# Kernel optimization log

Hardware: AMD Instinct MI355X
Metric: run time of the kernel (lower is better)

Reference implementation:

```python
import jax, jax.numpy as jnp
import numpy as np

N = 131072      # 8192 sudoku puzzles x 16 cells
E = 1048576     # random constraint edges (avg degree 8)
HID = 64
NEG_SLOPE = 0.2


def setup_inputs() -> dict:
    key = jax.random.key(0)
    ks = jax.random.split(key, 18)
    p = lambda k, shape: jax.random.normal(k, shape, dtype=jnp.float32) * 0.05
    return {
        "x": jax.random.randint(ks[0], (N,), 0, 5),
        "edge_index": jax.random.randint(ks[1], (2, E), 0, N),
        "emb": p(ks[2], (5, HID)),
        # conv1: in 64 -> heads=4, C=64, concat
        "W1": p(ks[3], (HID, 4 * HID)),
        "a1_src": p(ks[4], (4, HID)),
        "a1_dst": p(ks[5], (4, HID)),
        "b1": p(ks[6], (4 * HID,)),
        # conv2: in 256 -> heads=4, C=64, concat
        "W2": p(ks[7], (4 * HID, 4 * HID)),
        "a2_src": p(ks[8], (4, HID)),
        "a2_dst": p(ks[9], (4, HID)),
        "b2": p(ks[10], (4 * HID,)),
        # conv3: in 256 -> heads=1, C=64, no concat
        "W3": p(ks[11], (4 * HID, HID)),
        "a3_src": p(ks[12], (1, HID)),
        "a3_dst": p(ks[13], (1, HID)),
        "b3": p(ks[14], (HID,)),
        "fc_w": p(ks[15], (HID, 5)),
        "fc_b": p(ks[16], (5,)),
    }


def gat_conv(x, src, dst, W, a_src, a_dst, b, concat):
    """PyG-style GATConv (self-loops already appended to src/dst)."""
    n = x.shape[0]
    H, C = a_src.shape
    h = (x @ W).reshape(n, H, C)                       # [N,H,C]
    alpha_s = jnp.einsum('nhc,hc->nh', h, a_src)       # [N,H]
    alpha_d = jnp.einsum('nhc,hc->nh', h, a_dst)
    e = jax.nn.leaky_relu(alpha_s[src] + alpha_d[dst], NEG_SLOPE)  # [E,H]
    # scatter-softmax over incoming edges per destination node
    e_max = jax.ops.segment_max(e, dst, num_segments=n)
    e_exp = jnp.exp(e - e_max[dst])
    denom = jax.ops.segment_sum(e_exp, dst, num_segments=n)
    alpha = e_exp / (denom[dst] + 1e-16)               # [E,H]
    msg = h[src] * alpha[:, :, None]                   # [E,H,C]
    out = jax.ops.segment_sum(msg, dst, num_segments=n)  # [N,H,C]
    out = out.reshape(n, H * C) if concat else out.mean(axis=1)
    return out + b


def reference(x, edge_index, emb, W1, a1_src, a1_dst, b1,
              W2, a2_src, a2_dst, b2, W3, a3_src, a3_dst, b3, fc_w, fc_b):
    n = x.shape[0]
    loops = jnp.arange(n)
    src = jnp.concatenate([edge_index[0], loops])  # add self-loops (PyG default)
    dst = jnp.concatenate([edge_index[1], loops])
    h = emb[x]                                                    # [N,64]
    h = jax.nn.elu(gat_conv(h, src, dst, W1, a1_src, a1_dst, b1, True))
    h = jax.nn.elu(gat_conv(h, src, dst, W2, a2_src, a2_dst, b2, True))
    h = jax.nn.elu(gat_conv(h, src, dst, W3, a3_src, a3_dst, b3, False))
    return h @ fc_w + fc_b                                        # [N,5]
```

## Files before the change

### kernel.cpp

```cpp
#include <hip/hip_runtime.h>
#include <hip/hip_bf16.h>
#include <hip/hip_fp8.h>

typedef __attribute__((ext_vector_type(8))) short short8;
typedef __attribute__((ext_vector_type(4))) short short4_t;
typedef __attribute__((ext_vector_type(4))) float floatx4;
typedef __attribute__((ext_vector_type(2))) float floatx2;

constexpr int NB  = 256;
constexpr int CAP = 6144;

__device__ __forceinline__ unsigned short f2bf(float f){
  unsigned int u = __float_as_uint(f);
  u += 0x7FFF + ((u >> 16) & 1);
  return (unsigned short)(u >> 16);
}
__device__ __forceinline__ float bf2f(unsigned short h){
  return __uint_as_float(((unsigned int)h) << 16);
}
__device__ __forceinline__ float lrelu(float x){ return x > 0.f ? x : 0.2f * x; }
__device__ __forceinline__ float eluf(float x){ return x > 0.f ? x : (__expf(x) - 1.f); }

__device__ __forceinline__ unsigned char f2fp8(float f){
  __hip_fp8_e4m3 t(f);
  return (unsigned char)t.__x;
}
__device__ __forceinline__ float fp82f(unsigned char b){
  __hip_fp8_e4m3 t;
  t.__x = (__hip_fp8_storage_t)b;
  return (float)t;
}

template<bool HI>
__device__ __forceinline__ floatx2 fp8pk2(unsigned int v){
#if defined(__has_builtin) && __has_builtin(__builtin_amdgcn_cvt_pk_f32_fp8)
  return __builtin_amdgcn_cvt_pk_f32_fp8((int)v, HI);
#else
  floatx2 r;
  constexpr int sh = HI ? 16 : 0;
  r.x = fp82f((unsigned char)((v >> sh) & 0xFF));
  r.y = fp82f((unsigned char)((v >> (sh + 8)) & 0xFF));
  return r;
#endif
}

__device__ __forceinline__ unsigned int f32x4_to_fp8(float a0, float a1, float a2, float a3){
#if defined(__has_builtin) && __has_builtin(__builtin_amdgcn_cvt_pk_fp8_f32)
  int w = 0;
  w = __builtin_amdgcn_cvt_pk_fp8_f32(a0, a1, w, false);
  w = __builtin_amdgcn_cvt_pk_fp8_f32(a2, a3, w, true);
  return (unsigned int)w;
#else
  return (unsigned int)f2fp8(a0) | ((unsigned int)f2fp8(a1) << 8) |
         ((unsigned int)f2fp8(a2) << 16) | ((unsigned int)f2fp8(a3) << 24);
#endif
}

__device__ __forceinline__ int scr512(int p){
  int c = p >> 4, s = p & 15;
  int cc = ((c & 7) << 2) | (c >> 3);
  return (cc << 4) | s;
}

__device__ __forceinline__ void gload16(const unsigned short* g, unsigned short* l){
  __builtin_amdgcn_global_load_lds(
      (const __attribute__((address_space(1))) unsigned int*)(const void*)g,
      (__attribute__((address_space(3))) unsigned int*)(void*)l,
      16, 0, 0);
}

__global__ __launch_bounds__(256) void part_prep_k(const int* __restrict__ ei, int E, int shift,
                                                   const int* __restrict__ x,
                                                   int* __restrict__ gcnt,
                                                   unsigned* __restrict__ bbuf, int PB,
                                                   const float* __restrict__ W2,
                                                   unsigned short* __restrict__ Wp2,
                                                   const float* __restrict__ W3,
                                                   unsigned short* __restrict__ Wp3,
                                                   const float* __restrict__ emb,
                                                   const float* __restrict__ W1,
                                                   const float* __restrict__ a1s,
                                                   const float* __restrict__ a1d,
                                                   float* __restrict__ T1,
                                                   float* __restrict__ wt_tab){
  int blk = blockIdx.x;
  int tid = threadIdx.x;
  if (blk < PB){
    __shared__ int hist[NB];
    __shared__ int base[NB];
    hist[tid] = 0;
    __syncthreads();
    int blk_start = blk * 4096;
    int ldmask = (1 << shift) - 1;
    unsigned word[16];
    int bkt[16], lp[16];
    #pragma unroll
    for (int k = 0; k < 16; k++){
      int i = blk_start + k * 256 + tid;
      if (i < E){
        int dst = ei[E + i];
        int s = ei[i];
        int xs = x[s];
        bkt[k] = dst >> shift;
        word[k] = (unsigned)s | ((unsigned)(dst & ldmask) << 17) | ((unsigned)xs << 26);
        lp[k] = atomicAdd(&hist[bkt[k]], 1);
      } else {
        bkt[k] = -1;
      }
    }
    __syncthreads();
    base[tid] = atomicAdd(&gcnt[tid], hist[tid]);
    __syncthreads();
    #pragma unroll
    for (int k = 0; k < 16; k++){
      if (bkt[k] >= 0){
        int b = bkt[k];
        bbuf[(size_t)b * CAP + base[b] + lp[k]] = word[k];
      }
    }
    return;
  }
  int b = blk - PB;
  if (b < 256){
    int idx = b * 256 + tid;
    int k = idx >> 8, nn = idx & 255;
    Wp2[nn * 256 + k] = f2bf(W2[idx]);
  } else if (b < 320){
    int idx = (b - 256) * 256 + tid;
    int k = idx >> 6, nn = idx & 63;
    Wp3[nn * 256 + k] = f2bf(W3[idx]);
  } else {
    __shared__ float t_lds[1280];
    __shared__ float as_l[20], ad_l[20];
    for (int i = tid; i < 1280; i += 256){
      int r = i >> 8, c = i & 255;
      float s = 0.f;
      for (int k = 0; k < 64; k++) s += emb[r * 64 + k] * W1[k * 256 + c];
      t_lds[i] = s;
      T1[i] = s;
    }
    __syncthreads();
    if (tid < 20){
      int r = tid >> 2, hh = tid & 3;
      float ss = 0.f, sd = 0.f;
      for (int c = 0; c < 64; c++){
        float f = t_lds[r * 256 + hh * 64 + c];
        ss += f * a1s[hh * 64 + c];
        sd += f * a1d[hh * 64 + c];
      }
      as_l[tid] = ss;
      ad_l[tid] = sd;
    }
    __syncthreads();
    if (tid < 100){
      int xd = tid / 20, rest = tid % 20;
      int h = rest & 3;
      wt_tab[tid] = __expf(lrelu(as_l[rest] + ad_l[xd * 4 + h]));
    }
  }
}

__global__ __launch_bounds__(256) void bscan_k(const int* __restrict__ gcnt,
                                               int* __restrict__ gbase,
                                               int* __restrict__ row_ptr, int N, int dpb){
  __shared__ int s[NB];
  int t = threadIdx.x;
  int v = gcnt[t] + dpb;
  s[t] = v;
  __syncthreads();
  #pragma unroll
  for (int off = 1; off < NB; off <<= 1){
    int u = (t >= off) ? s[t - off] : 0;
    __syncthreads();
    s[t] += u;
    __syncthreads();
  }
  gbase[t] = s[t] - v;
  if (t == NB - 1){ gbase[NB] = s[t]; row_ptr[N] = s[t]; }
}

__global__ __launch_bounds__(256) void sort_k(const unsigned* __restrict__ bbuf,
                                              const int* __restrict__ gcnt,
                                              const int* __restrict__ gbase,
                                              const int* __restrict__ x,
                                              int* __restrict__ row_ptr,
                                              int* __restrict__ sorted_src,
                                              int* __restrict__ perm,
                                              uint2* __restrict__ cnt5, int dpb){
  __shared__ int counts[512];
  __shared__ int curs[512];
  __shared__ int wsum[256];
  __shared__ int sortedL[CAP + 512];
  __shared__ int dh[64];
  __shared__ int h5[512 * 5];
  int b = blockIdx.x, tid = threadIdx.x;
  int cnt = gcnt[b];
  int dstBase = b * dpb;
  int gb = gbase[b];
  counts[tid] = 0;
  counts[tid + 256] = 0;
  for (int i = tid; i < dpb * 5; i += 256) h5[i] = 0;
  __syncthreads();
  for (int i = tid; i < cnt; i += 256){
    unsigned pw = bbuf[(size_t)b * CAP + i];
    atomicAdd(&counts[(pw >> 17) & (dpb - 1)], 1);
  }
  {
    int x0 = x[dstBase + 2 * tid];
    int x1 = x[dstBase + 2 * tid + 1];
    atomicAdd(&h5[(2 * tid) * 5 + x0], 1);
    atomicAdd(&h5[(2 * tid + 1) * 5 + x1], 1);
  }
  __syncthreads();
  int c0 = counts[2 * tid] + 1;
  int c1 = counts[2 * tid + 1] + 1;
  int sum = c0 + c1;
  wsum[tid] = sum;
  __syncthreads();
  #pragma unroll
  for (int off = 1; off < 256; off <<= 1){
    int u = (tid >= off) ? wsum[tid - off] : 0;
    __syncthreads();
    wsum[tid] += u;
    __syncthreads();
  }
  int ex = wsum[tid] - sum;
  int ro0 = ex, ro1 = ex + c0;
  curs[2 * tid] = ro0 + 1;
  curs[2 * tid + 1] = ro1 + 1;
  sortedL[ro0] = dstBase + 2 * tid;
  sortedL[ro1] = dstBase + 2 * tid + 1;
  row_ptr[dstBase + 2 * tid] = gb + ro0;
  row_ptr[dstBase + 2 * tid + 1] = gb + ro1;
  __syncthreads();
  for (int i = tid; i < cnt; i += 256){
    unsigned pw = bbuf[(size_t)b * CAP + i];
    int ldst = (pw >> 17) & (dpb - 1);
    int pos = atomicAdd(&curs[ldst], 1);
    sortedL[pos] = (int)(pw & 0x1FFFF);
    atomicAdd(&h5[ldst * 5 + (pw >> 26)], 1);
  }
  __syncthreads();
  int tot = cnt + dpb;
  for (int i = tid; i < tot; i += 256) sorted_src[gb + i] = sortedL[i];

  {
    int d0 = 2 * tid, d1 = 2 * tid + 1;
    unsigned lo0 = (unsigned)h5[d0 * 5 + 0] | ((unsigned)h5[d0 * 5 + 1] << 8) |
                   ((unsigned)h5[d0 * 5 + 2] << 16) | ((unsigned)h5[d0 * 5 + 3] << 24);
    unsigned lo1 = (unsigned)h5[d1 * 5 + 0] | ((unsigned)h5[d1 * 5 + 1] << 8) |
                   ((unsigned)h5[d1 * 5 + 2] << 16) | ((unsigned)h5[d1 * 5 + 3] << 24);
    cnt5[dstBase + d0] = make_uint2(lo0, (unsigned)h5[d0 * 5 + 4]);
    cnt5[dstBase + d1] = make_uint2(lo1, (unsigned)h5[d1 * 5 + 4]);
  }

  __syncthreads();
  if (tid < 64) dh[tid] = 0;
  __syncthreads();
  int dg0 = c0 < 63 ? c0 : 63;
  int dg1 = c1 < 63 ? c1 : 63;
  int r0 = atomicAdd(&dh[dg0], 1);
  int r1 = atomicAdd(&dh[dg1], 1);
  __syncthreads();
  if (tid == 0){
    int run = 0;
    for (int i = 0; i < 64; i++){ int c = dh[i]; dh[i] = run; run += c; }
  }
  __syncthreads();
  perm[dstBase + scr512(dh[dg0] + r0)] = dstBase + 2 * tid;
  perm[dstBase + scr512(dh[dg1] + r1)] = dstBase + 2 * tid + 1;
}

template<int BN, int MODE, bool F8OUT>
__global__ __launch_bounds__(256) void gemm_lds_k(const unsigned short* __restrict__ A,
                                                  const unsigned short* __restrict__ Wp,
                                                  void* __restrict__ Cout, int Nc,
                                                  const float* __restrict__ a_src,
                                                  const float* __restrict__ a_dst,
                                                  float* __restrict__ as_arr,
                                                  float* __restrict__ ad_arr){
  constexpr int K = 256;
  constexpr int NT = BN / 32;
  __shared__ unsigned short Alds[128 * 32];
  __shared__ unsigned short Blds[BN * 32];
  __shared__ float asl[128], adl[128];
  __shared__ float pas[128][2], pad[128][2];
  int tid = threadIdx.x;
  int w = tid >> 6, l = tid & 63;
  int r16 = l & 15, quad = l >> 4;
  int wr = w >> 1, wc = w & 1;
  int mBase = blockIdx.x * 128;
  int nBase = blockIdx.y * BN;

  if constexpr (MODE == 1){
    if (tid < 128){ asl[tid] = a_src[nBase + tid]; adl[tid] = a_dst[nBase + tid]; }
  }
  if constexpr (MODE == 2){
    if (tid < 64){ asl[tid] = a_src[tid]; adl[tid] = a_dst[tid]; }
  }

  int arow = l >> 2;
  int kcol = (l & 3) * 8;
  const unsigned short* gA0 = A + (size_t)(mBase + w * 32 + arow) * K + kcol;
  const unsigned short* gA1 = gA0 + (size_t)16 * K;
  unsigned short* lA0 = &Alds[(w * 32) * 32];
  unsigned short* lA1 = &Alds[(w * 32 + 16) * 32];
  const unsigned short* gB0;
  const unsigned short* gB1 = nullptr;
  unsigned short* lB0;
  unsigned short* lB1 = nullptr;
  if constexpr (BN == 128){
    gB0 = Wp + (size_t)(nBase + w * 32 + arow) * K + kcol;
    gB1 = gB0 + (size_t)16 * K;
    lB0 = &Blds[(w * 32) * 32];
    lB1 = &Blds[(w * 32 + 16) * 32];
  } else {
    gB0 = Wp + (size_t)(nBase + w * 16 + arow) * K + kcol;
    lB0 = &Blds[(w * 16) * 32];
  }

  floatx4 acc[4][NT];
  #pragma unroll
  for (int mt = 0; mt < 4; mt++)
    #pragma unroll
    for (int nt = 0; nt < NT; nt++){ floatx4 z = {0.f,0.f,0.f,0.f}; acc[mt][nt] = z; }

  for (int kt = 0; kt < 8; kt++){
    int ko = kt * 32;
    gload16(gA0 + ko, lA0);
    gload16(gA1 + ko, lA1);
    gload16(gB0 + ko, lB0);
    if constexpr (BN == 128) gload16(gB1 + ko, lB1);
    __syncthreads();
    short8 af[4], bfr[NT];
    #pragma unroll
    for (int mt = 0; mt < 4; mt++)
      af[mt] = *(const short8*)&Alds[(wr * 64 + mt * 16 + r16) * 32 + quad * 8];
    #pragma unroll
    for (int nt = 0; nt < NT; nt++)
      bfr[nt] = *(const short8*)&Blds[(wc * (BN / 2) + nt * 16 + r16) * 32 + quad * 8];
    #pragma unroll
    for (int mt = 0; mt < 4; mt++)
      #pragma unroll
      for (int nt = 0; nt < NT; nt++)
        acc[mt][nt] = __builtin_amdgcn_mfma_f32_16x16x32_bf16(af[mt], bfr[nt], acc[mt][nt], 0, 0, 0);
    __syncthreads();
  }

  #pragma unroll
  for (int mt = 0; mt < 4; mt++){
    #pragma unroll
    for (int nt = 0; nt < NT; nt++){
      if constexpr (F8OUT){
        unsigned int pk = f32x4_to_fp8(acc[mt][nt][0] * 64.f, acc[mt][nt][1] * 64.f,
                                       acc[mt][nt][2] * 64.f, acc[mt][nt][3] * 64.f);
        int col = nBase + wc * (BN / 2) + nt * 16 + r16;
        int row0 = mBase + wr * 64 + mt * 16 + quad * 4;
        #pragma unroll
        for (int r = 0; r < 4; r++)
          ((unsigned char*)Cout)[(size_t)(row0 + r) * Nc + col] =
              (unsigned char)((pk >> (r * 8)) & 0xFF);
      } else {
        #pragma unroll
        for (int r = 0; r < 4; r++){
          int row = mBase + wr * 64 + mt * 16 + quad * 4 + r;
          int col = nBase + wc * (BN / 2) + nt * 16 + r16;
          ((unsigned short*)Cout)[(size_t)row * Nc + col] = f2bf(acc[mt][nt][r]);
        }
      }
    }
  }
  if constexpr (MODE == 1){
    int head = (nBase + wc * 64) >> 6;
    #pragma unroll
    for (int mt = 0; mt < 4; mt++){
      #pragma unroll
      for (int r = 0; r < 4; r++){
        float ps = 0.f, pd = 0.f;
        #pragma unroll
        for (int nt = 0; nt < NT; nt++){
          float v = acc[mt][nt][r];
          int ci = wc * 64 + nt * 16 + r16;
          ps += v * asl[ci];
          pd += v * adl[ci];
        }
        ps += __shfl_xor(ps, 1, 64); ps += __shfl_xor(ps, 2, 64);
        ps += __shfl_xor(ps, 4, 64); ps += __shfl_xor(ps, 8, 64);
        pd += __shfl_xor(pd, 1, 64); pd += __shfl_xor(pd, 2, 64);
        pd += __shfl_xor(pd, 4, 64); pd += __shfl_xor(pd, 8, 64);
        if (r16 == 0){
          int row = mBase + wr * 64 + mt * 16 + quad * 4 + r;
          as_arr[row * 4 + head] = ps;
          ad_arr[row * 4 + head] = pd;
        }
      }
    }
  }
  if constexpr (MODE == 2){
    #pragma unroll
    for (int mt = 0; mt < 4; mt++){
      #pragma unroll
      for (int r = 0; r < 4; r++){
        float ps = 0.f, pd = 0.f;
        #pragma unroll
        for (int nt = 0; nt < NT; nt++){
          float v = acc[mt][nt][r];
          int ci = wc * 32 + nt * 16 + r16;
          ps += v * asl[ci];
          pd += v * adl[ci];
        }
        ps += __shfl_xor(ps, 1, 64); ps += __shfl_xor(ps, 2, 64);
        ps += __shfl_xor(ps, 4, 64); ps += __shfl_xor(ps, 8, 64);
        pd += __shfl_xor(pd, 1, 64); pd += __shfl_xor(pd, 2, 64);
        pd += __shfl_xor(pd, 4, 64); pd += __shfl_xor(pd, 8, 64);
        if (r16 == 0){
          int lr = wr * 64 + mt * 16 + quad * 4 + r;
          pas[lr][wc] = ps;
          pad[lr][wc] = pd;
        }
      }
    }
    __syncthreads();
    if (tid < 128){
      as_arr[mBase + tid] = pas[tid][0] + pas[tid][1];
      ad_arr[mBase + tid] = pad[tid][0] + pad[tid][1];
    }
  }
}


__global__ __launch_bounds__(256) void agg1_k(const int* __restrict__ x,
                                              const float* __restrict__ T1,
                                              const float* __restrict__ wt_tab,
                                              const uint2* __restrict__ cnt5,
                                              const float* __restrict__ bias,
                                              unsigned short* __restrict__ outb){
  __shared__ float t_lds[1280];
  __shared__ float wt_l[100], b_lds[256];
  __shared__ float cnt_lds[256][5];
  __shared__ int xd_lds[256];
  int tid = threadIdx.x;
  for (int i = tid; i < 1280; i += 256) t_lds[i] = T1[i];
  if (tid < 100) wt_l[tid] = wt_tab[tid];
  b_lds[tid] = bias[tid];
  int d = blockIdx.x * 256 + tid;
  uint2 cw = cnt5[d];
  xd_lds[tid] = x[d];
  cnt_lds[tid][0] = (float)(cw.x & 0xFF);
  cnt_lds[tid][1] = (float)((cw.x >> 8) & 0xFF);
  cnt_lds[tid][2] = (float)((cw.x >> 16) & 0xFF);
  cnt_lds[tid][3] = (float)(cw.x >> 24);
  cnt_lds[tid][4] = (float)(cw.y & 0xFF);
  __syncthreads();
  int w = tid >> 6, l = tid & 63;
  int head = l >> 4;
  int c0i = l * 4;
  for (int dl = w; dl < 256; dl += 4){
    int dd = blockIdx.x * 256 + dl;
    int xd20 = xd_lds[dl] * 20;
    float ws[5];
    float den = 0.f;
    #pragma unroll
    for (int v2 = 0; v2 < 5; v2++){
      float wv = wt_l[xd20 + v2 * 4 + head] * cnt_lds[dl][v2];
      ws[v2] = wv;
      den += wv;
    }
    float inv = 1.f / (den + 1e-16f);
    float num[4] = {0.f, 0.f, 0.f, 0.f};
    #pragma unroll
    for (int v2 = 0; v2 < 5; v2++){
      const float4 row = *(const float4*)&t_lds[v2 * 256 + c0i];
      num[0] += ws[v2] * row.x;
      num[1] += ws[v2] * row.y;
      num[2] += ws[v2] * row.z;
      num[3] += ws[v2] * row.w;
    }
    short4_t ov;
    #pragma unroll
    for (int j = 0; j < 4; j++)
      ov[j] = (short)f2bf(eluf(num[j] * inv + b_lds[c0i + j]));
    *(short4_t*)(outb + (size_t)dd * 256 + c0i) = ov;
  }
}


__global__ __launch_bounds__(256) void agg4g_k(const unsigned char* __restrict__ h8,
                                               const float* __restrict__ as_arr,
                                               const float* __restrict__ ad_arr,
                                               const int* __restrict__ row_ptr,
                                               const int* __restrict__ sorted_src,
                                               const int* __restrict__ perm,
                                               const float* __restrict__ bias,
                                               const unsigned short* __restrict__ Wp3,
                                               const float* __restrict__ a3s,
                                               const float* __restrict__ a3d,
                                               unsigned char* __restrict__ h3out,
                                               float* __restrict__ as3,
                                               float* __restrict__ ad3){
  constexpr int LDK = 264;
  __shared__ unsigned short hlds[16 * LDK];
  __shared__ float pasl[16][4], padl[16][4];
  __shared__ unsigned char h3st[16 * 64];
  __shared__ int dlds[16];
  int tid = threadIdx.x;
  int w = tid >> 6, l = tid & 63;
  int g = l >> 4, q = l & 15;
  int rr = w * 4 + g;
  int d = perm[blockIdx.x * 16 + rr];
  if (q == 0) dlds[rr] = d;

  unsigned coff = (unsigned)(q * 16);
  int head = q >> 2;
  int start = row_ptr[d], end = row_ptr[d + 1];
  float a_d = ad_arr[d * 4 + head];
  floatx2 ac[8];
  #pragma unroll
  for (int j = 0; j < 8; j++){ floatx2 z = {0.f, 0.f}; ac[j] = z; }
  float den = 0.f;
  int e = start;
  for (; e + 3 < end; e += 4){
    unsigned s0 = (unsigned)sorted_src[e];
    unsigned s1 = (unsigned)sorted_src[e + 1];
    unsigned s2 = (unsigned)sorted_src[e + 2];
    unsigned s3 = (unsigned)sorted_src[e + 3];
    uint4 v0 = *(const uint4*)(h8 + (((size_t)s0 << 8) | coff));
    uint4 v1 = *(const uint4*)(h8 + (((size_t)s1 << 8) | coff));
    uint4 v2 = *(const uint4*)(h8 + (((size_t)s2 << 8) | coff));
    uint4 v3 = *(const uint4*)(h8 + (((size_t)s3 << 8) | coff));
    float w0 = __expf(lrelu(as_arr[(s0 << 2) + head] + a_d));
    float w1 = __expf(lrelu(as_arr[(s1 << 2) + head] + a_d));
    float w2 = __expf(lrelu(as_arr[(s2 << 2) + head] + a_d));
    float w3 = __expf(lrelu(as_arr[(s3 << 2) + head] + a_d));
    den += (w0 + w1) + (w2 + w3);
    floatx2 W0 = {w0, w0}, W1 = {w1, w1}, W2 = {w2, w2}, W3 = {w3, w3};
    ac[0] += W0 * fp8pk2<false>(v0.x) + W1 * fp8pk2<false>(v1.x)
           + W2 * fp8pk2<false>(v2.x) + W3 * fp8pk2<false>(v3.x);
    ac[1] += W0 * fp8pk2<true>(v0.x)  + W1 * fp8pk2<true>(v1.x)
           + W2 * fp8pk2<true>(v2.x)  + W3 * fp8pk2<true>(v3.x);
    ac[2] += W0 * fp8pk2<false>(v0.y) + W1 * fp8pk2<false>(v1.y)
           + W2 * fp8pk2<false>(v2.y) + W3 * fp8pk2<false>(v3.y);
    ac[3] += W0 * fp8pk2<true>(v0.y)  + W1 * fp8pk2<true>(v1.y)
           + W2 * fp8pk2<true>(v2.y)  + W3 * fp8pk2<true>(v3.y);
    ac[4] += W0 * fp8pk2<false>(v0.z) + W1 * fp8pk2<false>(v1.z)
           + W2 * fp8pk2<false>(v2.z) + W3 * fp8pk2<false>(v3.z);
    ac[5] += W0 * fp8pk2<true>(v0.z)  + W1 * fp8pk2<true>(v1.z)
           + W2 * fp8pk2<true>(v2.z)  + W3 * fp8pk2<true>(v3.z);
    ac[6] += W0 * fp8pk2<false>(v0.w) + W1 * fp8pk2<false>(v1.w)
           + W2 * fp8pk2<false>(v2.w) + W3 * fp8pk2<false>(v3.w);
    ac[7] += W0 * fp8pk2<true>(v0.w)  + W1 * fp8pk2<true>(v1.w)
           + W2 * fp8pk2<true>(v2.w)  + W3 * fp8pk2<true>(v3.w);
  }
  for (; e < end; e++){
    unsigned s = (unsigned)sorted_src[e];
    uint4 v = *(const uint4*)(h8 + (((size_t)s << 8) | coff));
    float wg = __expf(lrelu(as_arr[(s << 2) + head] + a_d));
    den += wg;
    floatx2 wv = {wg, wg};
    ac[0] += wv * fp8pk2<false>(v.x);
    ac[1] += wv * fp8pk2<true>(v.x);
    ac[2] += wv * fp8pk2<false>(v.y);
    ac[3] += wv * fp8pk2<true>(v.y);
    ac[4] += wv * fp8pk2<false>(v.z);
    ac[5] += wv * fp8pk2<true>(v.z);
    ac[6] += wv * fp8pk2<false>(v.w);
    ac[7] += wv * fp8pk2<true>(v.w);
  }
  float inv = 0.015625f / (den + 1e-16f);
  int cb = q * 16;
  float4 bv0 = *(const float4*)&bias[cb];
  float4 bv1 = *(const float4*)&bias[cb + 4];
  float4 bv2 = *(const float4*)&bias[cb + 8];
  float4 bv3 = *(const float4*)&bias[cb + 12];
  float bb[16] = {bv0.x, bv0.y, bv0.z, bv0.w, bv1.x, bv1.y, bv1.z, bv1.w,
                  bv2.x, bv2.y, bv2.z, bv2.w, bv3.x, bv3.y, bv3.z, bv3.w};
  short8 o0, o1;
  #pragma unroll
  for (int j = 0; j < 8; j++){
    float v = ((j & 1) ? ac[j >> 1].y : ac[j >> 1].x);
    o0[j] = (short)f2bf(eluf(v * inv + bb[j]));
  }
  #pragma unroll
  for (int j = 0; j < 8; j++){
    float v = ((j & 1) ? ac[4 + (j >> 1)].y : ac[4 + (j >> 1)].x);
    o1[j] = (short)f2bf(eluf(v * inv + bb[8 + j]));
  }
  *(short8*)&hlds[rr * LDK + cb] = o0;
  *(short8*)&hlds[rr * LDK + cb + 8] = o1;
  __syncthreads();

  int r16 = l & 15, quad = l >> 4;
  floatx4 acc3 = {0.f, 0.f, 0.f, 0.f};
  #pragma unroll
  for (int kt = 0; kt < 8; kt++){
    short8 af = *(const short8*)&hlds[r16 * LDK + kt * 32 + quad * 8];
    short8 bf = *(const short8*)&Wp3[(w * 16 + r16) * 256 + kt * 32 + quad * 8];
    acc3 = __builtin_amdgcn_mfma_f32_16x16x32_bf16(af, bf, acc3, 0, 0, 0);
  }
  float a3sv = a3s[w * 16 + r16];
  float a3dv = a3d[w * 16 + r16];
  float ps[4], pd[4];
  #pragma unroll
  for (int r = 0; r < 4; r++){
    ps[r] = acc3[r] * a3sv;
    pd[r] = acc3[r] * a3dv;
    ps[r] += __shfl_xor(ps[r], 1, 64); ps[r] += __shfl_xor(ps[r], 2, 64);
    ps[r] += __shfl_xor(ps[r], 4, 64); ps[r] += __shfl_xor(ps[r], 8, 64);
    pd[r] += __shfl_xor(pd[r], 1, 64); pd[r] += __shfl_xor(pd[r], 2, 64);
    pd[r] += __shfl_xor(pd[r], 4, 64); pd[r] += __shfl_xor(pd[r], 8, 64);
    h3st[(quad * 4 + r) * 64 + w * 16 + r16] = f2fp8(acc3[r] * 64.f);
  }
  if (r16 == 0){
    #pragma unroll
    for (int r = 0; r < 4; r++){
      pasl[quad * 4 + r][w] = ps[r];
      padl[quad * 4 + r][w] = pd[r];
    }
  }
  __syncthreads();
  {
    int row = tid >> 4, c4 = tid & 15;
    unsigned v = *(const unsigned*)&h3st[row * 64 + c4 * 4];
    int dd = dlds[row];
    *(unsigned*)(h3out + (size_t)dd * 64 + c4 * 4) = v;
    if (c4 == 0){
      as3[dd] = pasl[row][0] + pasl[row][1] + pasl[row][2] + pasl[row][3];
      ad3[dd] = padl[row][0] + padl[row][1] + padl[row][2] + padl[row][3];
    }
  }
}


__global__ __launch_bounds__(256) void agg3_k(const unsigned char* __restrict__ h8,
                                              const float* __restrict__ as_arr,
                                              const float* __restrict__ ad_arr,
                                              const int* __restrict__ row_ptr,
                                              const int* __restrict__ sorted_src,
                                              const int* __restrict__ perm,
                                              const float* __restrict__ bias,
                                              const float* __restrict__ fcw,
                                              const float* __restrict__ fcb,
                                              float* __restrict__ out){
  __shared__ float w_lds[320];
  __shared__ float fb5[5];
  int tid = threadIdx.x;
  for (int i = tid; i < 320; i += 256) w_lds[i] = fcw[i];
  if (tid < 5) fb5[tid] = fcb[tid];
  __syncthreads();
  int w = tid >> 6, l = tid & 63;
  int g = l >> 3, q = l & 7;
  int d = perm[blockIdx.x * 32 + w * 8 + g];
  unsigned coff = (unsigned)(q * 8);
  int start = row_ptr[d], end = row_ptr[d + 1];
  float a_d = ad_arr[d];
  floatx2 ac[4];
  #pragma unroll
  for (int j = 0; j < 4; j++){ floatx2 z = {0.f, 0.f}; ac[j] = z; }
  float den = 0.f;
  int e = start;
  for (; e + 3 < end; e += 4){
    unsigned s0 = (unsigned)sorted_src[e];
    unsigned s1 = (unsigned)sorted_src[e + 1];
    unsigned s2 = (unsigned)sorted_src[e + 2];
    unsigned s3 = (unsigned)sorted_src[e + 3];
    uint2 v0 = *(const uint2*)(h8 + (((size_t)s0 << 6) | coff));
    uint2 v1 = *(const uint2*)(h8 + (((size_t)s1 << 6) | coff));
    uint2 v2 = *(const uint2*)(h8 + (((size_t)s2 << 6) | coff));
    uint2 v3 = *(const uint2*)(h8 + (((size_t)s3 << 6) | coff));
    float w0 = __expf(lrelu(as_arr[s0] + a_d));
    float w1 = __expf(lrelu(as_arr[s1] + a_d));
    float w2 = __expf(lrelu(as_arr[s2] + a_d));
    float w3 = __expf(lrelu(as_arr[s3] + a_d));
    den += (w0 + w1) + (w2 + w3);
    floatx2 W0 = {w0, w0}, W1 = {w1, w1}, W2 = {w2, w2}, W3 = {w3, w3};
    ac[0] += W0 * fp8pk2<false>(v0.x) + W1 * fp8pk2<false>(v1.x)
           + W2 * fp8pk2<false>(v2.x) + W3 * fp8pk2<false>(v3.x);
    ac[1] += W0 * fp8pk2<true>(v0.x)  + W1 * fp8pk2<true>(v1.x)
           + W2 * fp8pk2<true>(v2.x)  + W3 * fp8pk2<true>(v3.x);
    ac[2] += W0 * fp8pk2<false>(v0.y) + W1 * fp8pk2<false>(v1.y)
           + W2 * fp8pk2<false>(v2.y) + W3 * fp8pk2<false>(v3.y);
    ac[3] += W0 * fp8pk2<true>(v0.y)  + W1 * fp8pk2<true>(v1.y)
           + W2 * fp8pk2<true>(v2.y)  + W3 * fp8pk2<true>(v3.y);
  }
  for (; e < end; e++){
    unsigned s = (unsigned)sorted_src[e];
    float wg = __expf(lrelu(as_arr[s] + a_d));
    den += wg;
    uint2 v = *(const uint2*)(h8 + (((size_t)s << 6) | coff));
    floatx2 wv = {wg, wg};
    ac[0] += wv * fp8pk2<false>(v.x);
    ac[1] += wv * fp8pk2<true>(v.x);
    ac[2] += wv * fp8pk2<false>(v.y);
    ac[3] += wv * fp8pk2<true>(v.y);
  }
  float inv = 0.015625f / (den + 1e-16f);
  int cb = q * 8;
  float4 bA = *(const float4*)&bias[cb];
  float4 bB = *(const float4*)&bias[cb + 4];
  float bb[8] = {bA.x, bA.y, bA.z, bA.w, bB.x, bB.y, bB.z, bB.w};
  float p0 = 0.f, p1 = 0.f, p2 = 0.f, p3 = 0.f, p4 = 0.f;
  #pragma unroll
  for (int j = 0; j < 8; j++){
    float v = ((j & 1) ? ac[j >> 1].y : ac[j >> 1].x);
    float h = eluf(v * inv + bb[j]);
    const float* wr = &w_lds[(cb + j) * 5];
    p0 += h * wr[0];
    p1 += h * wr[1];
    p2 += h * wr[2];
    p3 += h * wr[3];
    p4 += h * wr[4];
  }
  p0 += __shfl_xor(p0, 1, 64); p0 += __shfl_xor(p0, 2, 64); p0 += __shfl_xor(p0, 4, 64);
  p1 += __shfl_xor(p1, 1, 64); p1 += __shfl_xor(p1, 2, 64); p1 += __shfl_xor(p1, 4, 64);
  p2 += __shfl_xor(p2, 1, 64); p2 += __shfl_xor(p2, 2, 64); p2 += __shfl_xor(p2, 4, 64);
  p3 += __shfl_xor(p3, 1, 64); p3 += __shfl_xor(p3, 2, 64); p3 += __shfl_xor(p3, 4, 64);
  p4 += __shfl_xor(p4, 1, 64); p4 += __shfl_xor(p4, 2, 64); p4 += __shfl_xor(p4, 4, 64);
  if (q == 0){
    float* o = out + (size_t)d * 5;
    o[0] = p0 + fb5[0];
    o[1] = p1 + fb5[1];
    o[2] = p2 + fb5[2];
    o[3] = p3 + fb5[3];
    o[4] = p4 + fb5[4];
  }
}


extern "C" void kernel_launch(void* const* d_in, const int* in_sizes, int n_in,
                              void* d_out, int out_size, void* d_ws, size_t ws_size,
                              hipStream_t stream){
  const int*   x    = (const int*)d_in[0];
  const int*   ei   = (const int*)d_in[1];
  const float* emb  = (const float*)d_in[2];
  const float* W1   = (const float*)d_in[3];
  const float* a1s  = (const float*)d_in[4];
  const float* a1d  = (const float*)d_in[5];
  const float* b1   = (const float*)d_in[6];
  const float* W2   = (const float*)d_in[7];
  const float* a2s  = (const float*)d_in[8];
  const float* a2d  = (const float*)d_in[9];
  const float* b2   = (const float*)d_in[10];
  const float* W3   = (const float*)d_in[11];
  const float* a3s  = (const float*)d_in[12];
  const float* a3d  = (const float*)d_in[13];
  const float* b3   = (const float*)d_in[14];
  const float* fcw  = (const float*)d_in[15];
  const float* fcb  = (const float*)d_in[16];
  float* out = (float*)d_out;

  const int N = in_sizes[0];
  const int E = in_sizes[1] / 2;
  const int dpb = N / NB;
  int shift = 0;
  while ((1 << shift) < dpb) shift++;
  const int PB = (E + 4095) / 4096;

  char* base = (char*)d_ws;
  size_t off = 0;
  auto alloc = [&](size_t bytes) -> void* {
    void* p = base + off;
    off += (bytes + 255) & ~(size_t)255;
    return p;
  };
  unsigned short* bufB    = (unsigned short*)alloc((size_t)N * 256 * 2);
  unsigned char*  buf8    = (unsigned char*)alloc((size_t)N * 256);
  unsigned char*  buf8b   = (unsigned char*)alloc((size_t)N * 64);
  float* alpha_s          = (float*)alloc((size_t)N * 4 * 4);
  float* alpha_d          = (float*)alloc((size_t)N * 4 * 4);
  float* as3              = (float*)alloc((size_t)N * 4);
  float* ad3              = (float*)alloc((size_t)N * 4);
  int* row_ptr            = (int*)alloc((size_t)(N + 1) * 4);
  int* sorted_src         = (int*)alloc((size_t)(E + N) * 4);
  int* perm               = (int*)alloc((size_t)N * 4);
  uint2* cnt5             = (uint2*)alloc((size_t)N * 8);
  unsigned* bbuf          = (unsigned*)alloc((size_t)NB * CAP * 4);
  int* gcnt               = (int*)alloc((size_t)NB * 4);
  int* gbase              = (int*)alloc((size_t)(NB + 1) * 4);
  float* T1               = (float*)alloc(5 * 256 * 4);
  float* wt_tab           = (float*)alloc(100 * 4);
  unsigned short* Wp2     = (unsigned short*)alloc(256 * 256 * 2);
  unsigned short* Wp3     = (unsigned short*)alloc(64 * 256 * 2);

  (void)hipMemsetAsync(gcnt, 0, (size_t)NB * 4, stream);
  part_prep_k<<<PB + 321, 256, 0, stream>>>(ei, E, shift, x, gcnt, bbuf, PB,
                                            W2, Wp2, W3, Wp3, emb, W1, a1s, a1d, T1, wt_tab);
  bscan_k<<<1, 256, 0, stream>>>(gcnt, gbase, row_ptr, N, dpb);
  sort_k<<<NB, 256, 0, stream>>>(bbuf, gcnt, gbase, x, row_ptr, sorted_src, perm, cnt5, dpb);

  agg1_k<<<N / 256, 256, 0, stream>>>(x, T1, wt_tab, cnt5, b1, bufB);

  gemm_lds_k<128, 1, true><<<dim3(N / 128, 2), 256, 0, stream>>>(bufB, Wp2, buf8, 256,
                                                                 a2s, a2d, alpha_s, alpha_d);
  agg4g_k<<<N / 16, 256, 0, stream>>>(buf8, alpha_s, alpha_d, row_ptr, sorted_src, perm, b2,
                                      Wp3, a3s, a3d, buf8b, as3, ad3);

  agg3_k<<<N / 32, 256, 0, stream>>>(buf8b, as3, ad3, row_ptr, sorted_src, perm, b3,
                                     fcw, fcb, out);
}
```

Before: 327.2 us.

## Process 64 destination rows per block in fused layer-2 aggregation kernel

The fused aggregation plus layer-3 projection kernel now loops over four 16-row sub-tiles per block, launching a quarter as many blocks. The Wp3 weight fragments are loaded once into registers and reused across the four MFMA passes, and the bias loads and per-block overhead are amortised. Shared-memory use grows roughly fourfold, which may reduce occupancy for the latency-bound gather loop. The scr512 swizzle is also changed to permute 64-element chunks instead of 16-element chunks.

New measurement: 309.3 us (median of 2 runs). 1.06x faster.

```diff
diff --git a/kernel.cpp b/kernel.cpp
--- a/kernel.cpp
+++ b/kernel.cpp
@@ -57,9 +57,9 @@
 }
 
 __device__ __forceinline__ int scr512(int p){
-  int c = p >> 4, s = p & 15;
-  int cc = ((c & 7) << 2) | (c >> 3);
-  return (cc << 4) | s;
+  int c = p >> 6, s = p & 63;
+  int cc = ((c & 3) << 1) | (c >> 2);
+  return (cc << 6) | s;
 }
 
 __device__ __forceinline__ void gload16(const unsigned short* g, unsigned short* l){
@@ -499,74 +499,16 @@
                                                float* __restrict__ as3,
                                                float* __restrict__ ad3){
   constexpr int LDK = 264;
-  __shared__ unsigned short hlds[16 * LDK];
-  __shared__ float pasl[16][4], padl[16][4];
-  __shared__ unsigned char h3st[16 * 64];
-  __shared__ int dlds[16];
+  __shared__ unsigned short hlds[64 * LDK];
+  __shared__ float pasl[64][4], padl[64][4];
+  __shared__ unsigned char h3st[64 * 64];
+  __shared__ int dlds[64];
   int tid = threadIdx.x;
   int w = tid >> 6, l = tid & 63;
   int g = l >> 4, q = l & 15;
   int rr = w * 4 + g;
-  int d = perm[blockIdx.x * 16 + rr];
-  if (q == 0) dlds[rr] = d;
-
   unsigned coff = (unsigned)(q * 16);
   int head = q >> 2;
-  int start = row_ptr[d], end = row_ptr[d + 1];
-  float a_d = ad_arr[d * 4 + head];
-  floatx2 ac[8];
-  #pragma unroll
-  for (int j = 0; j < 8; j++){ floatx2 z = {0.f, 0.f}; ac[j] = z; }
-  float den = 0.f;
-  int e = start;
-  for (; e + 3 < end; e += 4){
-    unsigned s0 = (unsigned)sorted_src[e];
-    unsigned s1 = (unsigned)sorted_src[e + 1];
-    unsigned s2 = (unsigned)sorted_src[e + 2];
-    unsigned s3 = (unsigned)sorted_src[e + 3];
-    uint4 v0 = *(const uint4*)(h8 + (((size_t)s0 << 8) | coff));
-    uint4 v1 = *(const uint4*)(h8 + (((size_t)s1 << 8) | coff));
-    uint4 v2 = *(const uint4*)(h8 + (((size_t)s2 << 8) | coff));
-    uint4 v3 = *(const uint4*)(h8 + (((size_t)s3 << 8) | coff));
-    float w0 = __expf(lrelu(as_arr[(s0 << 2) + head] + a_d));
-    float w1 = __expf(lrelu(as_arr[(s1 << 2) + head] + a_d));
-    float w2 = __expf(lrelu(as_arr[(s2 << 2) + head] + a_d));
-    float w3 = __expf(lrelu(as_arr[(s3 << 2) + head] + a_d));
-    den += (w0 + w1) + (w2 + w3);
-    floatx2 W0 = {w0, w0}, W1 = {w1, w1}, W2 = {w2, w2}, W3 = {w3, w3};
-    ac[0] += W0 * fp8pk2<false>(v0.x) + W1 * fp8pk2<false>(v1.x)
-           + W2 * fp8pk2<false>(v2.x) + W3 * fp8pk2<false>(v3.x);
-    ac[1] += W0 * fp8pk2<true>(v0.x)  + W1 * fp8pk2<true>(v1.x)
-           + W2 * fp8pk2<true>(v2.x)  + W3 * fp8pk2<true>(v3.x);
-    ac[2] += W0 * fp8pk2<false>(v0.y) + W1 * fp8pk2<false>(v1.y)
-           + W2 * fp8pk2<false>(v2.y) + W3 * fp8pk2<false>(v3.y);
-    ac[3] += W0 * fp8pk2<true>(v0.y)  + W1 * fp8pk2<true>(v1.y)
-           + W2 * fp8pk2<true>(v2.y)  + W3 * fp8pk2<true>(v3.y);
-    ac[4] += W0 * fp8pk2<false>(v0.z) + W1 * fp8pk2<false>(v1.z)
-           + W2 * fp8pk2<false>(v2.z) + W3 * fp8pk2<false>(v3.z);
-    ac[5] += W0 * fp8pk2<true>(v0.z)  + W1 * fp8pk2<true>(v1.z)
-           + W2 * fp8pk2<true>(v2.z)  + W3 * fp8pk2<true>(v3.z);
-    ac[6] += W0 * fp8pk2<false>(v0.w) + W1 * fp8pk2<false>(v1.w)
-           + W2 * fp8pk2<false>(v2.w) + W3 * fp8pk2<false>(v3.w);
-    ac[7] += W0 * fp8pk2<true>(v0.w)  + W1 * fp8pk2<true>(v1.w)
-           + W2 * fp8pk2<true>(v2.w)  + W3 * fp8pk2<true>(v3.w);
-  }
-  for (; e < end; e++){
-    unsigned s = (unsigned)sorted_src[e];
-    uint4 v = *(const uint4*)(h8 + (((size_t)s << 8) | coff));
-    float wg = __expf(lrelu(as_arr[(s << 2) + head] + a_d));
-    den += wg;
-    floatx2 wv = {wg, wg};
-    ac[0] += wv * fp8pk2<false>(v.x);
-    ac[1] += wv * fp8pk2<true>(v.x);
-    ac[2] += wv * fp8pk2<false>(v.y);
-    ac[3] += wv * fp8pk2<true>(v.y);
-    ac[4] += wv * fp8pk2<false>(v.z);
-    ac[5] += wv * fp8pk2<true>(v.z);
-    ac[6] += wv * fp8pk2<false>(v.w);
-    ac[7] += wv * fp8pk2<true>(v.w);
-  }
-  float inv = 0.015625f / (den + 1e-16f);
   int cb = q * 16;
   float4 bv0 = *(const float4*)&bias[cb];
   float4 bv1 = *(const float4*)&bias[cb + 4];
@@ -574,52 +516,121 @@
   float4 bv3 = *(const float4*)&bias[cb + 12];
   float bb[16] = {bv0.x, bv0.y, bv0.z, bv0.w, bv1.x, bv1.y, bv1.z, bv1.w,
                   bv2.x, bv2.y, bv2.z, bv2.w, bv3.x, bv3.y, bv3.z, bv3.w};
-  short8 o0, o1;
+
+  for (int it = 0; it < 4; it++){
+    int row = it * 16 + rr;
+    int d = perm[blockIdx.x * 64 + row];
+    if (q == 0) dlds[row] = d;
+    int start = row_ptr[d], end = row_ptr[d + 1];
+    float a_d = ad_arr[d * 4 + head];
+    floatx2 ac[8];
+    #pragma unroll
+    for (int j = 0; j < 8; j++){ floatx2 z = {0.f, 0.f}; ac[j] = z; }
+    float den = 0.f;
+    int e = start;
+    for (; e + 3 < end; e += 4){
+      unsigned s0 = (unsigned)sorted_src[e];
+      unsigned s1 = (unsigned)sorted_src[e + 1];
+      unsigned s2 = (unsigned)sorted_src[e + 2];
+      unsigned s3 = (unsigned)sorted_src[e + 3];
+      uint4 v0 = *(const uint4*)(h8 + (((size_t)s0 << 8) | coff));
+      uint4 v1 = *(const uint4*)(h8 + (((size_t)s1 << 8) | coff));
+      uint4 v2 = *(const uint4*)(h8 + (((size_t)s2 << 8) | coff));
+      uint4 v3 = *(const uint4*)(h8 + (((size_t)s3 << 8) | coff));
+      float w0 = __expf(lrelu(as_arr[(s0 << 2) + head] + a_d));
+      float w1 = __expf(lrelu(as_arr[(s1 << 2) + head] + a_d));
+      float w2 = __expf(lrelu(as_arr[(s2 << 2) + head] + a_d));
+      float w3 = __expf(lrelu(as_arr[(s3 << 2) + head] + a_d));
+      den += (w0 + w1) + (w2 + w3);
+      floatx2 W0 = {w0, w0}, W1 = {w1, w1}, W2 = {w2, w2}, W3 = {w3, w3};
+      ac[0] += W0 * fp8pk2<false>(v0.x) + W1 * fp8pk2<false>(v1.x)
+             + W2 * fp8pk2<false>(v2.x) + W3 * fp8pk2<false>(v3.x);
+      ac[1] += W0 * fp8pk2<true>(v0.x)  + W1 * fp8pk2<true>(v1.x)
+             + W2 * fp8pk2<true>(v2.x)  + W3 * fp8pk2<true>(v3.x);
+      ac[2] += W0 * fp8pk2<false>(v0.y) + W1 * fp8pk2<false>(v1.y)
+             + W2 * fp8pk2<false>(v2.y) + W3 * fp8pk2<false>(v3.y);
+      ac[3] += W0 * fp8pk2<true>(v0.y)  + W1 * fp8pk2<true>(v1.y)
+             + W2 * fp8pk2<true>(v2.y)  + W3 * fp8pk2<true>(v3.y);
+      ac[4] += W0 * fp8pk2<false>(v0.z) + W1 * fp8pk2<false>(v1.z)
+             + W2 * fp8pk2<false>(v2.z) + W3 * fp8pk2<false>(v3.z);
+      ac[5] += W0 * fp8pk2<true>(v0.z)  + W1 * fp8pk2<true>(v1.z)
+             + W2 * fp8pk2<true>(v2.z)  + W3 * fp8pk2<true>(v3.z);
+      ac[6] += W0 * fp8pk2<false>(v0.w) + W1 * fp8pk2<false>(v1.w)
+             + W2 * fp8pk2<false>(v2.w) + W3 * fp8pk2<false>(v3.w);
+      ac[7] += W0 * fp8pk2<true>(v0.w)  + W1 * fp8pk2<true>(v1.w)
+             + W2 * fp8pk2<true>(v2.w)  + W3 * fp8pk2<true>(v3.w);
+    }
+    for (; e < end; e++){
+      unsigned s = (unsigned)sorted_src[e];
+      uint4 v = *(const uint4*)(h8 + (((size_t)s << 8) | coff));
+      float wg = __expf(lrelu(as_arr[(s << 2) + head] + a_d));
+      den += wg;
+      floatx2 wv = {wg, wg};
+      ac[0] += wv * fp8pk2<false>(v.x);
+      ac[1] += wv * fp8pk2<true>(v.x);
+      ac[2] += wv * fp8pk2<false>(v.y);
+      ac[3] += wv * fp8pk2<true>(v.y);
+      ac[4] += wv * fp8pk2<false>(v.z);
+      ac[5] += wv * fp8pk2<true>(v.z);
+      ac[6] += wv * fp8pk2<false>(v.w);
+      ac[7] += wv * fp8pk2<true>(v.w);
+    }
+    float inv = 0.015625f / (den + 1e-16f);
+    short8 o0, o1;
+    #pragma unroll
+    for (int j = 0; j < 8; j++){
+      float v = ((j & 1) ? ac[j >> 1].y : ac[j >> 1].x);
+      o0[j] = (short)f2bf(eluf(v * inv + bb[j]));
+    }
+    #pragma unroll
+    for (int j = 0; j < 8; j++){
+      float v = ((j & 1) ? ac[4 + (j >> 1)].y : ac[4 + (j >> 1)].x);
+      o1[j] = (short)f2bf(eluf(v * inv + bb[8 + j]));
+    }
+    *(short8*)&hlds[row * LDK + cb] = o0;
+    *(short8*)&hlds[row * LDK + cb + 8] = o1;
+  }
+  __syncthreads();
+
+  int r16 = l & 15, quad = l >> 4;
+  short8 bfr[8];
   #pragma unroll
-  for (int j = 0; j < 8; j++){
-    float v = ((j & 1) ? ac[j >> 1].y : ac[j >> 1].x);
-    o0[j] = (short)f2bf(eluf(v * inv + bb[j]));
-  }
-  #pragma unroll
-  for (int j = 0; j < 8; j++){
-    float v = ((j & 1) ? ac[4 + (j >> 1)].y : ac[4 + (j >> 1)].x);
-    o1[j] = (short)f2bf(eluf(v * inv + bb[8 + j]));
-  }
-  *(short8*)&hlds[rr * LDK + cb] = o0;
-  *(short8*)&hlds[rr * LDK + cb + 8] = o1;
-  __syncthreads();
-
-  int r16 = l & 15, quad = l >> 4;
-  floatx4 acc3 = {0.f, 0.f, 0.f, 0.f};
-  #pragma unroll
-  for (int kt = 0; kt < 8; kt++){
-    short8 af = *(const short8*)&hlds[r16 * LDK + kt * 32 + quad * 8];
-    short8 bf = *(const short8*)&Wp3[(w * 16 + r16) * 256 + kt * 32 + quad * 8];
-    acc3 = __builtin_amdgcn_mfma_f32_16x16x32_bf16(af, bf, acc3, 0, 0, 0);
-  }
+  for (int kt = 0; kt < 8; kt++)
+    bfr[kt] = *(const short8*)&Wp3[(w * 16 + r16) * 256 + kt * 32 + quad * 8];
   float a3sv = a3s[w * 16 + r16];
   float a3dv = a3d[w * 16 + r16];
-  float ps[4], pd[4];
   #pragma unroll
-  for (int r = 0; r < 4; r++){
-    ps[r] = acc3[r] * a3sv;
-    pd[r] = acc3[r] * a3dv;
-    ps[r] += __shfl_xor(ps[r], 1, 64); ps[r] += __shfl_xor(ps[r], 2, 64);
-    ps[r] += __shfl_xor(ps[r], 4, 64); ps[r] += __shfl_xor(ps[r], 8, 64);
-    pd[r] += __shfl_xor(pd[r], 1, 64); pd[r] += __shfl_xor(pd[r], 2, 64);
-    pd[r] += __shfl_xor(pd[r], 4, 64); pd[r] += __shfl_xor(pd[r], 8, 64);
-    h3st[(quad * 4 + r) * 64 + w * 16 + r16] = f2fp8(acc3[r] * 64.f);
-  }
-  if (r16 == 0){
+  for (int it = 0; it < 4; it++){
+    floatx4 acc3 = {0.f, 0.f, 0.f, 0.f};
+    #pragma unroll
+    for (int kt = 0; kt < 8; kt++){
+      short8 af = *(const short8*)&hlds[(it * 16 + r16) * LDK + kt * 32 + quad * 8];
+      acc3 = __builtin_amdgcn_mfma_f32_16x16x32_bf16(af, bfr[kt], acc3, 0, 0, 0);
+    }
+    float ps[4], pd[4];
     #pragma unroll
     for (int r = 0; r < 4; r++){
-      pasl[quad * 4 + r][w] = ps[r];
-      padl[quad * 4 + r][w] = pd[r];
-    }
-  }
-  __syncthreads();
-  {
-    int row = tid >> 4, c4 = tid & 15;
+      ps[r] = acc3[r] * a3sv;
+      pd[r] = acc3[r] * a3dv;
+      ps[r] += __shfl_xor(ps[r], 1, 64); ps[r] += __shfl_xor(ps[r], 2, 64);
+      ps[r] += __shfl_xor(ps[r], 4, 64); ps[r] += __shfl_xor(ps[r], 8, 64);
+      pd[r] += __shfl_xor(pd[r], 1, 64); pd[r] += __shfl_xor(pd[r], 2, 64);
+      pd[r] += __shfl_xor(pd[r], 4, 64); pd[r] += __shfl_xor(pd[r], 8, 64);
+      h3st[(it * 16 + quad * 4 + r) * 64 + w * 16 + r16] = f2fp8(acc3[r] * 64.f);
+    }
+    if (r16 == 0){
+      #pragma unroll
+      for (int r = 0; r < 4; r++){
+        pasl[it * 16 + quad * 4 + r][w] = ps[r];
+        padl[it * 16 + quad * 4 + r][w] = pd[r];
+      }
+    }
+  }
+  __syncthreads();
+  #pragma unroll
+  for (int k2 = 0; k2 < 4; k2++){
+    int idx = k2 * 256 + tid;
+    int row = idx >> 4, c4 = idx & 15;
     unsigned v = *(const unsigned*)&h3st[row * 64 + c4 * 4];
     int dd = dlds[row];
     *(unsigned*)(h3out + (size_t)dd * 64 + c4 * 4) = v;
@@ -791,7 +802,7 @@
 
   gemm_lds_k<128, 1, true><<<dim3(N / 128, 2), 256, 0, stream>>>(bufB, Wp2, buf8, 256,
                                                                  a2s, a2d, alpha_s, alpha_d);
-  agg4g_k<<<N / 16, 256, 0, stream>>>(buf8, alpha_s, alpha_d, row_ptr, sorted_src, perm, b2,
+  agg4g_k<<<N / 64, 256, 0, stream>>>(buf8, alpha_s, alpha_d, row_ptr, sorted_src, perm, b2,
                                       Wp3, a3s, a3d, buf8b, as3, ad3);
 
   agg3_k<<<N / 32, 256, 0, stream>>>(buf8b, as3, ad3, row_ptr, sorted_src, perm, b3,
```
